# Performance work log

Hardware: AMD Instinct MI355X
Metric: run time of the kernel (lower is better)

## Reference

```python
import jax, jax.numpy as jnp
import numpy as np

RADIUS = 1.0
NORM_ORD = 2.0
N_POINTS = 4194304


def _contract(p):
    # p: [..., 3] -> contracted points [..., 3] (MipNeRF-360 eq. 10)
    eps = jnp.finfo(p.dtype).eps
    mag = jnp.linalg.norm(p, ord=NORM_ORD, axis=-1)
    mag = jnp.maximum(mag, eps)
    norm_factor = (2.0 - RADIUS / mag) / mag
    mask = (mag <= RADIUS)[..., None]
    return jnp.where(mask, p / RADIUS, norm_factor[..., None] * p)


def setup_inputs() -> dict:
    key = jax.random.key(0)
    x = jax.random.normal(key, (N_POINTS, 3), dtype=jnp.float32) * 2.0
    return {"x": x, "output_jacobian": 1}


def reference(x, output_jacobian):
    x_contr = _contract(x)
    if output_jacobian:
        # per-point 3x3 jacobian, mirroring torch.func.vmap(jacrev(contract))
        jacobian = jax.vmap(jax.jacrev(_contract))(x.reshape(-1, x.shape[-1]))
        jacobian = jacobian.reshape(x.shape[:-1] + (x.shape[-1], x.shape[-1]))
        return (x_contr, jacobian)
    return x_contr
```

## Files before the change

kernel.cpp:

```cpp
#include <hip/hip_runtime.h>


typedef float v4f __attribute__((ext_vector_type(4)));

constexpr int BLOCK = 256;
constexpr int PPT   = 4;
constexpr int PPB   = BLOCK * PPT;

__global__ __launch_bounds__(BLOCK) void contract_jac_kernel(
    const float* __restrict__ x,
    float* __restrict__ out,
    long long n_points)
{
    const long long t = (long long)blockIdx.x * BLOCK + threadIdx.x;

    const v4f* x4 = reinterpret_cast<const v4f*>(x) + 3 * t;
    v4f a = x4[0], b = x4[1], c = x4[2];

    float px[PPT] = {a.x, a.w, b.z, c.y};
    float py[PPT] = {a.y, b.x, b.w, c.z};
    float pz[PPT] = {a.z, b.y, c.x, c.w};

    float s[PPT], cf[PPT];
    #pragma unroll
    for (int k = 0; k < PPT; ++k) {
        float m2   = fmaf(px[k], px[k], fmaf(py[k], py[k], pz[k] * pz[k]));
        float invm = rsqrtf(m2);
        float m    = m2 * invm;
        float sv   = (2.0f - invm) * invm;
        float i2   = invm * invm;
        float cv   = 2.0f * (1.0f - m) * (i2 * i2);
        bool inside = (m2 <= 1.0f);
        s[k]  = inside ? 1.0f : sv;
        cf[k] = inside ? 0.0f : cv;
    }

    v4f* oc = reinterpret_cast<v4f*>(out) + 3 * t;
    v4f o0 = {s[0] * px[0], s[0] * py[0], s[0] * pz[0], s[1] * px[1]};
    v4f o1 = {s[1] * py[1], s[1] * pz[1], s[2] * px[2], s[2] * py[2]};
    v4f o2 = {s[2] * pz[2], s[3] * px[3], s[3] * py[3], s[3] * pz[3]};
    oc[0] = o0; oc[1] = o1; oc[2] = o2;

    float j[PPT * 9];
    #pragma unroll
    for (int k = 0; k < PPT; ++k) {
        float cx = cf[k] * px[k];
        float cy = cf[k] * py[k];
        float cz = cf[k] * pz[k];
        float xy = cx * py[k];
        float xz = cx * pz[k];
        float yz = cy * pz[k];
        float* J = j + 9 * k;
        J[0] = fmaf(cx, px[k], s[k]);
        J[1] = xy;
        J[2] = xz;
        J[3] = xy;
        J[4] = fmaf(cy, py[k], s[k]);
        J[5] = yz;
        J[6] = xz;
        J[7] = yz;
        J[8] = fmaf(cz, pz[k], s[k]);
    }

    v4f* oj = reinterpret_cast<v4f*>(out + n_points * 3) + 9 * t;
    #pragma unroll
    for (int i = 0; i < 9; ++i) {
        v4f v = {j[4*i + 0], j[4*i + 1], j[4*i + 2], j[4*i + 3]};
        oj[i] = v;
    }
}

extern "C" void kernel_launch(void* const* d_in, const int* in_sizes, int n_in,
                              void* d_out, int out_size, void* d_ws, size_t ws_size,
                              hipStream_t stream) {
    const float* x = (const float*)d_in[0];
    float* out = (float*)d_out;

    long long n = in_sizes[0] / 3;
    int grid = (int)(n / PPB);

    contract_jac_kernel<<<grid, BLOCK, 0, stream>>>(x, out, n);
}
```

Before: 269.0 us.

## Stage outputs through shared memory for coalesced block-wide vector stores

Each thread now handles one point instead of four. It writes the contracted point and the 3x3 Jacobian into a shared-memory tile, and after a barrier the block writes the tile out as contiguous float4 stores. The aim is to replace the strided per-thread 16-byte stores, where each thread wrote 48 or 144 contiguous bytes, with fully coalesced stores. The cost is shared-memory traffic, a __syncthreads, scalar strided input loads, and four times as many blocks.

```diff
diff --git a/kernel.cpp b/kernel.cpp
--- a/kernel.cpp
+++ b/kernel.cpp
@@ -4,69 +4,60 @@
 typedef float v4f __attribute__((ext_vector_type(4)));
 
 constexpr int BLOCK = 256;
-constexpr int PPT   = 4;
-constexpr int PPB   = BLOCK * PPT;
 
 __global__ __launch_bounds__(BLOCK) void contract_jac_kernel(
     const float* __restrict__ x,
     float* __restrict__ out,
     long long n_points)
 {
-    const long long t = (long long)blockIdx.x * BLOCK + threadIdx.x;
+    __shared__ alignas(16) float st[BLOCK * 12];
 
-    const v4f* x4 = reinterpret_cast<const v4f*>(x) + 3 * t;
-    v4f a = x4[0], b = x4[1], c = x4[2];
+    const int tid = threadIdx.x;
+    const long long q0 = (long long)blockIdx.x * BLOCK;
 
-    float px[PPT] = {a.x, a.w, b.z, c.y};
-    float py[PPT] = {a.y, b.x, b.w, c.z};
-    float pz[PPT] = {a.z, b.y, c.x, c.w};
+    const float* p = x + 3 * (q0 + tid);
+    float px = p[0], py = p[1], pz = p[2];
 
-    float s[PPT], cf[PPT];
+    float m2   = fmaf(px, px, fmaf(py, py, pz * pz));
+    float invm = rsqrtf(m2);
+    float m    = m2 * invm;
+    float sv   = (2.0f - invm) * invm;
+    float i2   = invm * invm;
+    float cv   = 2.0f * (1.0f - m) * (i2 * i2);
+    bool inside = (m2 <= 1.0f);
+    float s  = inside ? 1.0f : sv;
+    float cf = inside ? 0.0f : cv;
+
+    float* sc = st + 3 * tid;
+    sc[0] = s * px;
+    sc[1] = s * py;
+    sc[2] = s * pz;
+
+    float cx = cf * px, cy = cf * py, cz = cf * pz;
+    float xy = cx * py, xz = cx * pz, yz = cy * pz;
+    float* sj = st + BLOCK * 3 + 9 * tid;
+    sj[0] = fmaf(cx, px, s);
+    sj[1] = xy;
+    sj[2] = xz;
+    sj[3] = xy;
+    sj[4] = fmaf(cy, py, s);
+    sj[5] = yz;
+    sj[6] = xz;
+    sj[7] = yz;
+    sj[8] = fmaf(cz, pz, s);
+
+    __syncthreads();
+
+    const v4f* st4 = reinterpret_cast<const v4f*>(st);
+    v4f* oc = reinterpret_cast<v4f*>(out + 3 * q0);
+    v4f* oj = reinterpret_cast<v4f*>(out + 3 * n_points + 9 * q0);
+
     #pragma unroll
-    for (int k = 0; k < PPT; ++k) {
-        float m2   = fmaf(px[k], px[k], fmaf(py[k], py[k], pz[k] * pz[k]));
-        float invm = rsqrtf(m2);
-        float m    = m2 * invm;
-        float sv   = (2.0f - invm) * invm;
-        float i2   = invm * invm;
-        float cv   = 2.0f * (1.0f - m) * (i2 * i2);
-        bool inside = (m2 <= 1.0f);
-        s[k]  = inside ? 1.0f : sv;
-        cf[k] = inside ? 0.0f : cv;
-    }
-
-    v4f* oc = reinterpret_cast<v4f*>(out) + 3 * t;
-    v4f o0 = {s[0] * px[0], s[0] * py[0], s[0] * pz[0], s[1] * px[1]};
-    v4f o1 = {s[1] * py[1], s[1] * pz[1], s[2] * px[2], s[2] * py[2]};
-    v4f o2 = {s[2] * pz[2], s[3] * px[3], s[3] * py[3], s[3] * pz[3]};
-    oc[0] = o0; oc[1] = o1; oc[2] = o2;
-
-    float j[PPT * 9];
-    #pragma unroll
-    for (int k = 0; k < PPT; ++k) {
-        float cx = cf[k] * px[k];
-        float cy = cf[k] * py[k];
-        float cz = cf[k] * pz[k];
-        float xy = cx * py[k];
-        float xz = cx * pz[k];
-        float yz = cy * pz[k];
-        float* J = j + 9 * k;
-        J[0] = fmaf(cx, px[k], s[k]);
-        J[1] = xy;
-        J[2] = xz;
-        J[3] = xy;
-        J[4] = fmaf(cy, py[k], s[k]);
-        J[5] = yz;
-        J[6] = xz;
-        J[7] = yz;
-        J[8] = fmaf(cz, pz[k], s[k]);
-    }
-
-    v4f* oj = reinterpret_cast<v4f*>(out + n_points * 3) + 9 * t;
-    #pragma unroll
-    for (int i = 0; i < 9; ++i) {
-        v4f v = {j[4*i + 0], j[4*i + 1], j[4*i + 2], j[4*i + 3]};
-        oj[i] = v;
+    for (int i = 0; i < 3; ++i) {
+        int g = tid + i * BLOCK;
+        v4f v = st4[g];
+        if (g < 192) oc[g] = v;
+        else         oj[g - 192] = v;
     }
 }
 
@@ -77,7 +68,7 @@
     float* out = (float*)d_out;
 
     long long n = in_sizes[0] / 3;
-    int grid = (int)(n / PPB);
+    int grid = (int)(n / BLOCK);
 
     contract_jac_kernel<<<grid, BLOCK, 0, stream>>>(x, out, n);
 }
```

Result: faster. 236.5 us (-12.1%).
